# Kernel optimization log

Hardware: AMD Instinct MI355X
Metric: run time of the kernel (lower is better)

Reference implementation:

```python
import jax, jax.numpy as jnp
import numpy as np

B, N, IN_C, HEAD_C, H, EXPAND, OUT_C = 4, 2048, 256, 32, 8, 1024, 256
QKV_DIM = HEAD_C * H * 2 + IN_C * H  # 2560
LN_EPS = 1e-5


def setup_inputs() -> dict:
    key = jax.random.key(0)
    ks = jax.random.split(key, 6)
    s = lambda fan: 1.0 / np.sqrt(fan)
    return {
        "x": jax.random.normal(ks[0], (B, N, IN_C), jnp.float32),
        "ln1_g": jnp.ones((IN_C,), jnp.float32),
        "ln1_b": jnp.zeros((IN_C,), jnp.float32),
        "Wqkv": jax.random.normal(ks[1], (IN_C, QKV_DIM), jnp.float32) * s(IN_C),
        "bqkv": jnp.zeros((QKV_DIM,), jnp.float32),
        "Wm": jax.random.normal(ks[2], (IN_C * H, IN_C), jnp.float32) * s(IN_C * H),
        "bm": jnp.zeros((IN_C,), jnp.float32),
        "ln2_g": jnp.ones((IN_C,), jnp.float32),
        "ln2_b": jnp.zeros((IN_C,), jnp.float32),
        "W1": jax.random.normal(ks[3], (IN_C, EXPAND), jnp.float32) * s(IN_C),
        "b1": jnp.zeros((EXPAND,), jnp.float32),
        "W2": jax.random.normal(ks[4], (EXPAND, OUT_C), jnp.float32) * s(EXPAND),
        "b2": jnp.zeros((OUT_C,), jnp.float32),
    }


def _ln(x, g, b):
    m = x.mean(-1, keepdims=True)
    v = jnp.mean(jnp.square(x - m), axis=-1, keepdims=True)
    return (x - m) * jax.lax.rsqrt(v + LN_EPS) * g + b


def reference(x, ln1_g, ln1_b, Wqkv, bqkv, Wm, bm, ln2_g, ln2_b, W1, b1, W2, b2):
    scale = HEAD_C ** -0.5
    qkv = _ln(x, ln1_g, ln1_b) @ Wqkv + bqkv  # [B,N,QKV_DIM]
    q, k, v = jnp.split(qkv, [HEAD_C * H, 2 * HEAD_C * H], axis=-1)
    q = q.reshape(B, N, H, HEAD_C)  # H-major channel split, matches einops
    k = k.reshape(B, N, H, HEAD_C)
    v = v.reshape(B, N, H, IN_C)    # NOTE: V has in_c channels per head
    attn = jax.nn.softmax(jnp.einsum('bnhc,bmhc->bhnm', q, k) * scale, axis=-1)
    out = jnp.einsum('bhnm,bmhc->bnhc', attn, v).reshape(B, N, H * IN_C)
    x = x + out @ Wm + bm  # residual + merge-head projection
    h = jax.nn.gelu(_ln(x, ln2_g, ln2_b) @ W1 + b1, approximate=False)
    return (h @ W2 + b2) + x  # shortcut is Identity (in_c == out_c)
```

## Files before the change

### kernel.cpp

```cpp
#include <hip/hip_runtime.h>
#include <hip/hip_bf16.h>

typedef unsigned short u16;
typedef __attribute__((ext_vector_type(8))) short bf8_t;
typedef __attribute__((ext_vector_type(4))) float f4_t;
typedef __attribute__((ext_vector_type(16))) float fx16;

__device__ __forceinline__ float bf2f(u16 v) {
    union { unsigned u; float f; } c; c.u = ((unsigned)v) << 16; return c.f;
}
__device__ __forceinline__ u16 f2bf(float f) {
    union { float f; unsigned u; } c; c.f = f;
    unsigned r = 0x7FFFu + ((c.u >> 16) & 1u);
    return (u16)((c.u + r) >> 16);
}
__device__ __forceinline__ u16 f2bf_hw(float f) {
    union { __hip_bfloat16 b; u16 u; } c; c.b = __float2bfloat16(f); return c.u;
}

#define B_   4
#define N_   2048
#define INC  256
#define H_   8
#define ROWS 8192

#define SEG_X     0
#define SEG_LN1G  2097152
#define SEG_LN1B  2097408
#define SEG_WQKV  2097664
#define SEG_BQKV  2753024
#define SEG_WM    2755584
#define SEG_BM    3279872
#define SEG_LN2G  3280128
#define SEG_LN2B  3280384
#define SEG_W1    3280640
#define SEG_B1    3542784
#define SEG_W2    3543808
#define SEG_B2    3805952
#define SEG_TOT   3806208

__device__ __forceinline__ int sniff_flag(const void* x0, int t, int* sh) {
    if (t == 0) *sh = 0;
    __syncthreads();
    int bad = 0;
    #pragma unroll
    for (int k2 = 0; k2 < 4; ++k2) {
        float v = bf2f(((const u16*)x0)[t * 4 + k2]);
        if (!(fabsf(v) < 1e10f)) bad = 1;
    }
    if (bad) atomicOr(sh, 1);
    __syncthreads();
    return *sh;
}

__global__ __launch_bounds__(256) void prep_k(
    const void* p0, const void* p1, const void* p2, const void* p3, const void* p4,
    const void* p5, const void* p6, const void* p7, const void* p8, const void* p9,
    const void* p10, const void* p11, const void* p12,
    u16* __restrict__ dst, u16* __restrict__ y, int* __restrict__ mkz)
{
    const int t = threadIdx.x;
    const int blk = blockIdx.x;
    __shared__ int sflag;
    const int flag = sniff_flag(p0, t, &sflag);

    if (blk < 8192) {
        const int i = blk * 256 + t;
        float v = flag ? ((const float*)p0)[i] : bf2f(((const u16*)p0)[i]);
        dst[i] = f2bf_hw(v);
        float s = v, s2 = v * v;
        #pragma unroll
        for (int d = 1; d < 64; d <<= 1) {
            s  += __shfl_xor(s,  d, 64);
            s2 += __shfl_xor(s2, d, 64);
        }
        __shared__ float rs[8];
        int w = t >> 6;
        if ((t & 63) == 0) { rs[w] = s; rs[4 + w] = s2; }
        __syncthreads();
        s  = rs[0] + rs[1] + rs[2] + rs[3];
        s2 = rs[4] + rs[5] + rs[6] + rs[7];
        float mean = s * (1.0f / INC);
        float var  = s2 * (1.0f / INC) - mean * mean;
        float inv  = rsqrtf(var + 1e-5f);
        float g  = flag ? ((const float*)p1)[t] : bf2f(((const u16*)p1)[t]);
        float bb = flag ? ((const float*)p2)[t] : bf2f(((const u16*)p2)[t]);
        y[i] = f2bf_hw((v - mean) * inv * g + bb);
        return;
    }

    if (blk < 8210) {
        if (blk == 8192 && t < 32) mkz[t] = 0;
        const int elem = (blk - 8192) * 256 + t;
        const void* p; int j; size_t doff;
        if      (elem < 2560) { p = p4;  j = elem;        doff = SEG_BQKV + j; }
        else if (elem < 2816) { p = p6;  j = elem - 2560; doff = SEG_BM   + j; }
        else if (elem < 3072) { p = p7;  j = elem - 2816; doff = SEG_LN2G + j; }
        else if (elem < 3328) { p = p8;  j = elem - 3072; doff = SEG_LN2B + j; }
        else if (elem < 4352) { p = p10; j = elem - 3328; doff = SEG_B1   + j; }
        else                  { p = p12; j = elem - 4352; doff = SEG_B2   + j; }
        dst[doff] = flag ? f2bf(((const float*)p)[j]) : ((const u16*)p)[j];
        return;
    }

    const int blk2 = blk - 8210;
    const void* W; int Kd, Nd, kt, nt; size_t seg;
    if (blk2 < 160)      { W = p3;  Kd = 256;  Nd = 2560; kt = blk2 / 40;  nt = blk2 % 40;  seg = SEG_WQKV; }
    else if (blk2 < 288) { int i2 = blk2 - 160; W = p5;  Kd = 2048; Nd = 256;  kt = i2 >> 2;  nt = i2 & 3;  seg = SEG_WM; }
    else if (blk2 < 352) { int i2 = blk2 - 288; W = p9;  Kd = 256;  Nd = 1024; kt = i2 >> 4;  nt = i2 & 15; seg = SEG_W1; }
    else                 { int i2 = blk2 - 352; W = p11; Kd = 1024; Nd = 256;  kt = i2 >> 2;  nt = i2 & 3;  seg = SEG_W2; }
    const int k0 = kt * 64, n0 = nt * 64;

    __shared__ u16 Tl[64][66];
    #pragma unroll
    for (int p = 0; p < 16; ++p) {
        int idx = t + p * 256;
        int r = idx >> 6, c = idx & 63;
        size_t si = (size_t)(k0 + r) * Nd + n0 + c;
        Tl[r][c] = flag ? f2bf(((const float*)W)[si]) : ((const u16*)W)[si];
    }
    __syncthreads();
    u16* dp = dst + seg;
    #pragma unroll
    for (int p = 0; p < 8; ++p) {
        int idx = t + p * 256;
        int rn = idx >> 5, ck = (idx & 31) * 2;
        ushort2 v; v.x = Tl[ck][rn]; v.y = Tl[ck + 1][rn];
        *(ushort2*)(dp + (size_t)(n0 + rn) * Kd + k0 + ck) = v;
    }
}

template<bool BF16IN>
__global__ __launch_bounds__(256) void ln_k(const void* __restrict__ xp,
        const u16* __restrict__ g, const u16* __restrict__ b, u16* __restrict__ y)
{
    int row  = blockIdx.x * 4 + (threadIdx.x >> 6);
    int lane = threadIdx.x & 63;
    int c0   = lane * 4;
    float v[4];
    if (BF16IN) {
        ushort4 u = *(const ushort4*)((const u16*)xp + (size_t)row * INC + c0);
        v[0] = bf2f(u.x); v[1] = bf2f(u.y); v[2] = bf2f(u.z); v[3] = bf2f(u.w);
    } else {
        float4 f = *(const float4*)((const float*)xp + (size_t)row * INC + c0);
        v[0] = f.x; v[1] = f.y; v[2] = f.z; v[3] = f.w;
    }
    float s = v[0] + v[1] + v[2] + v[3];
    float s2 = v[0]*v[0] + v[1]*v[1] + v[2]*v[2] + v[3]*v[3];
    #pragma unroll
    for (int d = 1; d < 64; d <<= 1) {
        s  += __shfl_xor(s,  d, 64);
        s2 += __shfl_xor(s2, d, 64);
    }
    float mean = s * (1.0f / INC);
    float var  = s2 * (1.0f / INC) - mean * mean;
    float inv  = rsqrtf(var + 1e-5f);
    ushort4 gv = *(const ushort4*)(g + c0);
    ushort4 bv = *(const ushort4*)(b + c0);
    ushort4 o;
    o.x = f2bf_hw((v[0] - mean) * inv * bf2f(gv.x) + bf2f(bv.x));
    o.y = f2bf_hw((v[1] - mean) * inv * bf2f(gv.y) + bf2f(bv.y));
    o.z = f2bf_hw((v[2] - mean) * inv * bf2f(gv.z) + bf2f(bv.z));
    o.w = f2bf_hw((v[3] - mean) * inv * bf2f(gv.w) + bf2f(bv.w));
    *(ushort4*)(y + (size_t)row * INC + c0) = o;
}

enum { EP_QKV = 0, EP_MERGE = 1, EP_GELU = 2, EP_FFN2 = 3 };

template<int MODE>
__global__ __launch_bounds__(256) void gemm_big(
    const u16* __restrict__ A, const u16* __restrict__ Bt,
    const u16* __restrict__ bias, void* __restrict__ outp,
    u16* __restrict__ qh, u16* __restrict__ kh, u16* __restrict__ vh,
    int* __restrict__ mkz, int N, int K)
{
    const int t = threadIdx.x;
    const int w = t >> 6, lane = t & 63;
    const int l15 = lane & 15, quad = lane >> 4;
    const int col0 = blockIdx.x * 64;
    const int row0 = blockIdx.y * 256;
    const int mrow = row0 + w * 64;

    __shared__ u16 Tsu[256 * 72];

    const u16* Ap = A  + (size_t)(mrow + l15) * K + quad * 8;
    const u16* Bp = Bt + (size_t)(col0 + l15) * K + quad * 8;

    f4_t acc[4][4];
    #pragma unroll
    for (int mi = 0; mi < 4; ++mi)
        #pragma unroll
        for (int ni = 0; ni < 4; ++ni)
            acc[mi][ni] = (f4_t){0.f, 0.f, 0.f, 0.f};

    for (int k0 = 0; k0 < K; k0 += 32) {
        bf8_t a[4], bb[4];
        #pragma unroll
        for (int mi = 0; mi < 4; ++mi)
            a[mi] = *(const bf8_t*)(Ap + (size_t)mi * 16 * K + k0);
        #pragma unroll
        for (int ni = 0; ni < 4; ++ni)
            bb[ni] = *(const bf8_t*)(Bp + (size_t)ni * 16 * K + k0);
        #pragma unroll
        for (int ni = 0; ni < 4; ++ni)
            #pragma unroll
            for (int mi = 0; mi < 4; ++mi)
                acc[mi][ni] = __builtin_amdgcn_mfma_f32_16x16x32_bf16(
                    a[mi], bb[ni], acc[mi][ni], 0, 0, 0);
    }

    if (MODE == EP_QKV) {
        if (col0 >= 512) {
            u16 (*Ts)[268] = (u16(*)[268])Tsu;
            #pragma unroll
            for (int mi = 0; mi < 4; ++mi)
                #pragma unroll
                for (int ni = 0; ni < 4; ++ni) {
                    float bz = bf2f(bias[col0 + ni * 16 + l15]);
                    #pragma unroll
                    for (int r = 0; r < 4; ++r)
                        Ts[ni * 16 + l15][w * 64 + mi * 16 + quad * 4 + r] =
                            f2bf_hw(acc[mi][ni][r] + bz);
                }
            __syncthreads();
            int vcg = col0 - 512;
            int hh  = vcg >> 8;
            int bb2 = row0 >> 11, nb = row0 & 2047;
            int bhh = bb2 * 8 + hh;
            int tok4 = t & 3, cl = (t >> 2) & 63;
            int vc = (vcg & 255) + cl;
            #pragma unroll
            for (int kb = 0; kb < 16; ++kb) {
                u16* dp = vh + (((size_t)bhh * 128 + ((nb >> 4) + kb)) * 256 + vc) * 16 + tok4 * 4;
                *(ushort4*)dp = *(const ushort4*)&Ts[cl][kb * 16 + tok4 * 4];
            }
        } else if (col0 < 256) {
            #pragma unroll
            for (int mi = 0; mi < 4; ++mi)
                #pragma unroll
                for (int r = 0; r < 4; ++r) {
                    int rg = mrow + mi * 16 + quad * 4 + r;
                    int bb2 = rg >> 11, n = rg & 2047;
                    #pragma unroll
                    for (int ni = 0; ni < 4; ++ni) {
                        int col = col0 + ni * 16 + l15;
                        float v = acc[mi][ni][r] + bf2f(bias[col]);
                        qh[(((size_t)(bb2 * 8 + (col >> 5))) * 2048 + n) * 32 + (col & 31)] = f2bf_hw(v);
                    }
                }
        } else {
            const int hA  = (col0 - 256) >> 5;
            const int bb2 = row0 >> 11;
            float mxA = 0.f, mxB = 0.f;
            #pragma unroll
            for (int mi = 0; mi < 4; ++mi)
                #pragma unroll
                for (int r = 0; r < 4; ++r) {
                    int rg = mrow + mi * 16 + quad * 4 + r;
                    int n = rg & 2047;
                    float vv[4];
                    #pragma unroll
                    for (int ni = 0; ni < 4; ++ni) {
                        int col = col0 + ni * 16 + l15;
                        float v = acc[mi][ni][r] + bf2f(bias[col]);
                        vv[ni] = v;
                        int c2 = col - 256;
                        int hd = c2 >> 5, ch = c2 & 31;
                        kh[(((size_t)(bb2 * 8 + hd) * 64 + (n >> 5)) * 2 + (ch >> 4)) * 512
                           + (n & 31) * 16 + (ch & 15)] = f2bf_hw(v);
                    }
                    float sA = vv[0] * vv[0] + vv[1] * vv[1];
                    float sB = vv[2] * vv[2] + vv[3] * vv[3];
                    #pragma unroll
                    for (int d = 1; d < 16; d <<= 1) {
                        sA += __shfl_xor(sA, d, 64);
                        sB += __shfl_xor(sB, d, 64);
                    }
                    mxA = fmaxf(mxA, sA);
                    mxB = fmaxf(mxB, sB);
                }
            if ((lane & 15) == 0) {
                atomicMax(mkz + bb2 * 8 + hA,     __float_as_int(mxA));
                atomicMax(mkz + bb2 * 8 + hA + 1, __float_as_int(mxB));
            }
        }
    } else {
        u16 (*Ts2)[72] = (u16(*)[72])Tsu;
        float bz[4];
        #pragma unroll
        for (int ni = 0; ni < 4; ++ni) bz[ni] = bf2f(bias[col0 + ni * 16 + l15]);
        #pragma unroll
        for (int mi = 0; mi < 4; ++mi)
            #pragma unroll
            for (int ni = 0; ni < 4; ++ni)
                #pragma unroll
                for (int r = 0; r < 4; ++r) {
                    float v = acc[mi][ni][r] + bz[ni];
                    v = 0.5f * v * (1.0f + erff(v * 0.70710678118654752f));
                    Ts2[w * 64 + mi * 16 + quad * 4 + r][ni * 16 + l15] = f2bf_hw(v);
                }
        __syncthreads();
        const int rl0 = t >> 3, c8 = (t & 7) * 8;
        #pragma unroll
        for (int p = 0; p < 8; ++p) {
            int rl = rl0 + p * 32;
            *(bf8_t*)((u16*)outp + (size_t)(row0 + rl) * N + col0 + c8) =
                *(const bf8_t*)&Ts2[rl][c8];
        }
    }
}

template<int MODE>
__global__ __launch_bounds__(256) void gemm_mfma(
    const u16* __restrict__ A, const u16* __restrict__ Bt,
    const u16* __restrict__ bias, const void* __restrict__ res,
    void* __restrict__ outp, int N, int K)
{
    const int t = threadIdx.x;
    const int w = t >> 6, lane = t & 63;
    const int l15 = lane & 15, quad = lane >> 4;
    const int col0 = blockIdx.x * 64;
    const int row0 = blockIdx.y * 128;
    const int mrow = row0 + w * 32;

    __shared__ float Tf[128][68];

    const u16* Ap = A  + (size_t)(mrow + l15) * K + quad * 8;
    const u16* Bp = Bt + (size_t)(col0 + l15) * K + quad * 8;

    f4_t acc[2][4];
    #pragma unroll
    for (int mi = 0; mi < 2; ++mi)
        #pragma unroll
        for (int ni = 0; ni < 4; ++ni)
            acc[mi][ni] = (f4_t){0.f, 0.f, 0.f, 0.f};

    for (int k0 = 0; k0 < K; k0 += 64) {
        bf8_t a[2][2], bb[4][2];
        #pragma unroll
        for (int kc = 0; kc < 2; ++kc) {
            #pragma unroll
            for (int mi = 0; mi < 2; ++mi)
                a[mi][kc] = *(const bf8_t*)(Ap + (size_t)mi * 16 * K + k0 + kc * 32);
            #pragma unroll
            for (int ni = 0; ni < 4; ++ni)
                bb[ni][kc] = *(const bf8_t*)(Bp + (size_t)ni * 16 * K + k0 + kc * 32);
        }
        #pragma unroll
        for (int kc = 0; kc < 2; ++kc)
            #pragma unroll
            for (int ni = 0; ni < 4; ++ni)
                #pragma unroll
                for (int mi = 0; mi < 2; ++mi)
                    acc[mi][ni] = __builtin_amdgcn_mfma_f32_16x16x32_bf16(
                        a[mi][kc], bb[ni][kc], acc[mi][ni], 0, 0, 0);
    }

    float bz[4];
    #pragma unroll
    for (int ni = 0; ni < 4; ++ni) bz[ni] = bf2f(bias[col0 + ni * 16 + l15]);
    #pragma unroll
    for (int mi = 0; mi < 2; ++mi)
        #pragma unroll
        for (int ni = 0; ni < 4; ++ni)
            #pragma unroll
            for (int r = 0; r < 4; ++r)
                Tf[w * 32 + mi * 16 + quad * 4 + r][ni * 16 + l15] = acc[mi][ni][r] + bz[ni];
    __syncthreads();

    const int rl0 = t >> 4, c4 = (t & 15) * 4;
    #pragma unroll
    for (int p = 0; p < 8; ++p) {
        int rl = rl0 + p * 16;
        float4 v = *(const float4*)&Tf[rl][c4];
        size_t base = (size_t)(row0 + rl) * N + col0 + c4;
        if (MODE == EP_MERGE) {
            ushort4 rv = *(const ushort4*)((const u16*)res + base);
            v.x += bf2f(rv.x); v.y += bf2f(rv.y); v.z += bf2f(rv.z); v.w += bf2f(rv.w);
        } else {
            float4 rv = *(const float4*)((const float*)res + base);
            v.x += rv.x; v.y += rv.y; v.z += rv.z; v.w += rv.w;
        }
        *(float4*)((float*)outp + base) = v;
    }
}

__global__ __launch_bounds__(256) void attn_k(
    const u16* __restrict__ qh, const u16* __restrict__ kh,
    const u16* __restrict__ vhT, const float* __restrict__ mk2,
    u16* __restrict__ ao)
{
    const int t = threadIdx.x;
    const int w = t >> 6, lane = t & 63;
    const int l31 = lane & 31, hi = lane >> 5;
    const int id = blockIdx.x;
    const int qt = (id >> 3) & 31;
    const int bh = (id >> 8) * 8 + (id & 7);
    const int b  = bh >> 3, h = bh & 7;
    const int n0 = qt * 64;
    const float SCALE = 0.17677669529663687f;
    const int sw = (l31 & 7) << 4;

    __shared__ __align__(16) u16 Pb[2][64][128];
    __shared__ float lds_l[4][64];
    __shared__ float lds_t[64];

    bf8_t qf[2][2];
    #pragma unroll
    for (int m = 0; m < 2; ++m)
        #pragma unroll
        for (int ks = 0; ks < 2; ++ks)
            qf[m][ks] = *(const bf8_t*)(qh + ((size_t)bh * 2048 + n0 + m * 32 + l31) * 32
                                        + ks * 16 + hi * 8);

    float mrow[2];
    #pragma unroll
    for (int m = 0; m < 2; ++m) {
        float q2 = 0.f;
        #pragma unroll
        for (int ks = 0; ks < 2; ++ks)
            #pragma unroll
            for (int i = 0; i < 8; ++i) {
                float qv = bf2f((u16)qf[m][ks][i]); q2 += qv * qv;
            }
        q2 += __shfl_xor(q2, 32, 64);
        mrow[m] = SCALE * sqrtf(q2 * mk2[bh]);
    }

    fx16 acc[2][2];
    #pragma unroll
    for (int a1 = 0; a1 < 2; ++a1)
        #pragma unroll
        for (int a2 = 0; a2 < 2; ++a2)
            #pragma unroll
            for (int e = 0; e < 16; ++e) acc[a1][a2][e] = 0.f;
    float lsum[2] = {0.f, 0.f};

    fx16 z16;
    #pragma unroll
    for (int e = 0; e < 16; ++e) z16[e] = 0.f;

    auto finish = [&](const fx16& s, int m, int g, char* base) {
        float p0 = __expf(fmaf(s[4 * g + 0], SCALE, -mrow[m]));
        float p1 = __expf(fmaf(s[4 * g + 1], SCALE, -mrow[m]));
        float p2 = __expf(fmaf(s[4 * g + 2], SCALE, -mrow[m]));
        float p3 = __expf(fmaf(s[4 * g + 3], SCALE, -mrow[m]));
        lsum[m] += (p0 + p1) + (p2 + p3);
        ushort4 pk;
        pk.x = f2bf_hw(p0); pk.y = f2bf_hw(p1); pk.z = f2bf_hw(p2); pk.w = f2bf_hw(p3);
        *(ushort4*)(base + (m * 32 + l31) * 256 + ((w * 64 + 16 * g + 8 * hi) ^ sw)) = pk;
    };

    bf8_t kA0, kA1;
    auto ldK = [&](int c) {
        const u16* kp = kh + ((size_t)bh * 64 + c * 4 + w) * 1024 + l31 * 16 + hi * 8;
        kA0 = *(const bf8_t*)kp;
        kA1 = *(const bf8_t*)(kp + 512);
    };

    {
        ldK(0);
        fx16 sA = __builtin_amdgcn_mfma_f32_32x32x16_bf16(kA0, qf[0][0], z16, 0, 0, 0);
        sA = __builtin_amdgcn_mfma_f32_32x32x16_bf16(kA1, qf[0][1], sA, 0, 0, 0);
        fx16 sB = __builtin_amdgcn_mfma_f32_32x32x16_bf16(kA0, qf[1][0], z16, 0, 0, 0);
        sB = __builtin_amdgcn_mfma_f32_32x32x16_bf16(kA1, qf[1][1], sB, 0, 0, 0);
        ldK(1);
        char* base0 = (char*)&Pb[0][0][0];
        #pragma unroll
        for (int g = 0; g < 4; ++g) finish(sA, 0, g, base0);
        #pragma unroll
        for (int g = 0; g < 4; ++g) finish(sB, 1, g, base0);
    }

    const u16* vpb = vhT + (((size_t)bh * 128) * 256 + w * 64 + l31) * 16 + hi * 8;
    bf8_t vb0 = *(const bf8_t*)vpb;
    bf8_t vb1 = *(const bf8_t*)(vpb + 512);

    int buf = 0;
    for (int c = 0; c < 16; ++c, buf ^= 1) {
        __syncthreads();
        const bool qn = (c < 15);
        fx16 sA, sB;
        if (qn) {
            sA = __builtin_amdgcn_mfma_f32_32x32x16_bf16(kA0, qf[0][0], z16, 0, 0, 0);
            sA = __builtin_amdgcn_mfma_f32_32x32x16_bf16(kA1, qf[0][1], sA, 0, 0, 0);
        }
        const char* pb = (const char*)&Pb[buf][0][0];
        char* wr = (char*)&Pb[buf ^ 1][0][0];
        const u16* vp = vpb + (size_t)c * 32768;
        #pragma unroll
        for (int ks = 0; ks < 8; ++ks) {
            bf8_t nv0 = *(const bf8_t*)(vp + (ks + 1) * 4096);
            bf8_t nv1 = *(const bf8_t*)(vp + (ks + 1) * 4096 + 512);
            bf8_t pa0 = *(const bf8_t*)(pb + l31 * 256        + ((ks * 32 + hi * 16) ^ sw));
            bf8_t pa1 = *(const bf8_t*)(pb + (32 + l31) * 256 + ((ks * 32 + hi * 16) ^ sw));
            __builtin_amdgcn_s_setprio(1);
            acc[0][0] = __builtin_amdgcn_mfma_f32_32x32x16_bf16(pa0, vb0, acc[0][0], 0, 0, 0);
            acc[0][1] = __builtin_amdgcn_mfma_f32_32x32x16_bf16(pa0, vb1, acc[0][1], 0, 0, 0);
            acc[1][0] = __builtin_amdgcn_mfma_f32_32x32x16_bf16(pa1, vb0, acc[1][0], 0, 0, 0);
            acc[1][1] = __builtin_amdgcn_mfma_f32_32x32x16_bf16(pa1, vb1, acc[1][1], 0, 0, 0);
            __builtin_amdgcn_s_setprio(0);
            if (qn) {
                if (ks < 4) {
                    finish(sA, 0, ks, wr);
                    if (ks == 3) {
                        sB = __builtin_amdgcn_mfma_f32_32x32x16_bf16(kA0, qf[1][0], z16, 0, 0, 0);
                        sB = __builtin_amdgcn_mfma_f32_32x32x16_bf16(kA1, qf[1][1], sB, 0, 0, 0);
                        if (c < 14) ldK(c + 2);
                    }
                } else {
                    finish(sB, 1, ks - 4, wr);
                }
            }
            vb0 = nv0; vb1 = nv1;
        }
    }

    #pragma unroll
    for (int m = 0; m < 2; ++m) {
        lsum[m] += __shfl_xor(lsum[m], 32, 64);
        if (hi == 0) lds_l[w][m * 32 + l31] = lsum[m];
    }
    __syncthreads();
    if (t < 64) lds_t[t] = lds_l[0][t] + lds_l[1][t] + lds_l[2][t] + lds_l[3][t];
    __syncthreads();

    #pragma unroll
    for (int mt = 0; mt < 2; ++mt)
        #pragma unroll
        for (int g = 0; g < 4; ++g) {
            f4_t lv = *(const f4_t*)&lds_t[mt * 32 + 8 * g + 4 * hi];
            #pragma unroll
            for (int j = 0; j < 4; ++j) {
                float inv = 1.0f / lv[j];
                int q = mt * 32 + 8 * g + 4 * hi + j;
                size_t rowbase = ((size_t)(b * 2048 + n0 + q)) * 2048 + h * 256 + w * 64;
                #pragma unroll
                for (int nt = 0; nt < 2; ++nt)
                    ao[rowbase + nt * 32 + l31] = f2bf_hw(acc[mt][nt][g * 4 + j] * inv);
            }
        }
}

extern "C" void kernel_launch(void* const* d_in, const int* in_sizes, int n_in,
                              void* d_out, int out_size, void* d_ws, size_t ws_size,
                              hipStream_t stream)
{
    u16* wsu = (u16*)d_ws;
    float* mk = (float*)(wsu + 64);

    const size_t CVT0 = 128;
    const size_t Y0   = CVT0 + SEG_TOT;
    const size_t QH0  = Y0  + 2097152;
    const size_t KH0  = QH0 + 2097152;
    const size_t VT0  = KH0 + 2097152;
    const size_t AO0  = VT0 + 16777216;
    const size_t X20  = AO0 + 16777216;

    u16* cvt = wsu + CVT0;
    u16* y   = wsu + Y0;
    u16* qh  = wsu + QH0;
    u16* kh  = wsu + KH0;
    u16* vhT = wsu + VT0;
    u16* ao  = wsu + AO0;
    float* x2 = (float*)(wsu + X20);
    u16* hbb  = wsu + AO0;

    const u16* xc   = cvt + SEG_X;
    const u16* Wqkv = cvt + SEG_WQKV;
    const u16* bqkv = cvt + SEG_BQKV;
    const u16* Wm   = cvt + SEG_WM;
    const u16* bm   = cvt + SEG_BM;
    const u16* ln2g = cvt + SEG_LN2G;
    const u16* ln2b = cvt + SEG_LN2B;
    const u16* W1   = cvt + SEG_W1;
    const u16* b1   = cvt + SEG_B1;
    const u16* W2   = cvt + SEG_W2;
    const u16* b2   = cvt + SEG_B2;

    prep_k<<<8626, 256, 0, stream>>>(
        d_in[0], d_in[1], d_in[2], d_in[3], d_in[4], d_in[5], d_in[6],
        d_in[7], d_in[8], d_in[9], d_in[10], d_in[11], d_in[12],
        cvt, y, (int*)mk);

    gemm_big<EP_QKV><<<dim3(2560 / 64, ROWS / 256), 256, 0, stream>>>(
        y, Wqkv, bqkv, nullptr, qh, kh, vhT, (int*)mk, 2560, 256);
    attn_k<<<1024, 256, 0, stream>>>(qh, kh, vhT, mk, ao);
    gemm_mfma<EP_MERGE><<<dim3(256 / 64, ROWS / 128), 256, 0, stream>>>(
        ao, Wm, bm, xc, x2, 256, 2048);
    ln_k<false><<<ROWS / 4, 256, 0, stream>>>(x2, ln2g, ln2b, y);
    gemm_big<EP_GELU><<<dim3(1024 / 64, ROWS / 256), 256, 0, stream>>>(
        y, W1, b1, hbb, nullptr, nullptr, nullptr, nullptr, 1024, 256);
    gemm_mfma<EP_FFN2><<<dim3(256 / 64, ROWS / 128), 256, 0, stream>>>(
        hbb, W2, b2, x2, d_out, 256, 1024);
}
```

Measured before the change: 331.2 us.

## Stage GEMM operand tiles in LDS via direct global-to-LDS loads with swizzle

Both GEMM kernels now load A and B tiles cooperatively into shared memory with global_load_lds (16-byte direct loads) using an XOR swizzle, then read MFMA fragments from LDS. Previously each wave loaded its fragments straight from global memory, so the B tile was fetched redundantly by every wave. The change aims to cut redundant global traffic and improve coalescing. In exchange it adds two barriers per K step with no double buffering, so load latency is not overlapped with compute.

```diff
diff --git a/kernel.cpp b/kernel.cpp
--- a/kernel.cpp
+++ b/kernel.cpp
@@ -16,6 +16,12 @@
 }
 __device__ __forceinline__ u16 f2bf_hw(float f) {
     union { __hip_bfloat16 b; u16 u; } c; c.b = __float2bfloat16(f); return c.u;
+}
+
+typedef __attribute__((address_space(3))) unsigned as3_u32;
+typedef __attribute__((address_space(1))) const unsigned as1_u32;
+__device__ __forceinline__ void gl16(const u16* g, u16* l) {
+    __builtin_amdgcn_global_load_lds((as1_u32*)(const void*)g, (as3_u32*)(void*)l, 16, 0, 0);
 }
 
 #define B_   4
@@ -179,12 +185,12 @@
     const int l15 = lane & 15, quad = lane >> 4;
     const int col0 = blockIdx.x * 64;
     const int row0 = blockIdx.y * 256;
-    const int mrow = row0 + w * 64;
-
-    __shared__ u16 Tsu[256 * 72];
-
-    const u16* Ap = A  + (size_t)(mrow + l15) * K + quad * 8;
-    const u16* Bp = Bt + (size_t)(col0 + l15) * K + quad * 8;
+    const int lr = lane >> 3;
+    const int sc = ((lane & 7) ^ lr) * 8;
+
+    __shared__ __align__(16) u16 Sb[20480];
+    u16* Al = Sb;
+    u16* Bl = Sb + 16384;
 
     f4_t acc[4][4];
     #pragma unroll
@@ -193,25 +199,42 @@
         for (int ni = 0; ni < 4; ++ni)
             acc[mi][ni] = (f4_t){0.f, 0.f, 0.f, 0.f};
 
-    for (int k0 = 0; k0 < K; k0 += 32) {
-        bf8_t a[4], bb[4];
-        #pragma unroll
-        for (int mi = 0; mi < 4; ++mi)
-            a[mi] = *(const bf8_t*)(Ap + (size_t)mi * 16 * K + k0);
-        #pragma unroll
-        for (int ni = 0; ni < 4; ++ni)
-            bb[ni] = *(const bf8_t*)(Bp + (size_t)ni * 16 * K + k0);
-        #pragma unroll
-        for (int ni = 0; ni < 4; ++ni)
-            #pragma unroll
-            for (int mi = 0; mi < 4; ++mi)
-                acc[mi][ni] = __builtin_amdgcn_mfma_f32_16x16x32_bf16(
-                    a[mi], bb[ni], acc[mi][ni], 0, 0, 0);
-    }
+    for (int k0 = 0; k0 < K; k0 += 64) {
+        #pragma unroll
+        for (int i = 0; i < 8; ++i) {
+            int r = w * 64 + i * 8;
+            gl16(A + (size_t)(row0 + r + lr) * K + k0 + sc, Al + r * 64);
+        }
+        gl16(Bt + (size_t)(col0 + w * 16 + lr) * K + k0 + sc,     Bl + (w * 16) * 64);
+        gl16(Bt + (size_t)(col0 + w * 16 + 8 + lr) * K + k0 + sc, Bl + (w * 16 + 8) * 64);
+        __syncthreads();
+        #pragma unroll
+        for (int kc = 0; kc < 2; ++kc) {
+            bf8_t a[4], bb[4];
+            #pragma unroll
+            for (int mi = 0; mi < 4; ++mi) {
+                int row = w * 64 + mi * 16 + l15;
+                a[mi] = *(const bf8_t*)(Al + row * 64 + ((kc * 4 + quad) ^ (row & 7)) * 8);
+            }
+            #pragma unroll
+            for (int ni = 0; ni < 4; ++ni) {
+                int row = ni * 16 + l15;
+                bb[ni] = *(const bf8_t*)(Bl + row * 64 + ((kc * 4 + quad) ^ (row & 7)) * 8);
+            }
+            #pragma unroll
+            for (int ni = 0; ni < 4; ++ni)
+                #pragma unroll
+                for (int mi = 0; mi < 4; ++mi)
+                    acc[mi][ni] = __builtin_amdgcn_mfma_f32_16x16x32_bf16(
+                        a[mi], bb[ni], acc[mi][ni], 0, 0, 0);
+        }
+        __syncthreads();
+    }
+    const int mrow = row0 + w * 64;
 
     if (MODE == EP_QKV) {
         if (col0 >= 512) {
-            u16 (*Ts)[268] = (u16(*)[268])Tsu;
+            u16 (*Ts)[268] = (u16(*)[268])Sb;
             #pragma unroll
             for (int mi = 0; mi < 4; ++mi)
                 #pragma unroll
@@ -285,7 +308,7 @@
             }
         }
     } else {
-        u16 (*Ts2)[72] = (u16(*)[72])Tsu;
+        u16 (*Ts2)[72] = (u16(*)[72])Sb;
         float bz[4];
         #pragma unroll
         for (int ni = 0; ni < 4; ++ni) bz[ni] = bf2f(bias[col0 + ni * 16 + l15]);
@@ -321,12 +344,13 @@
     const int l15 = lane & 15, quad = lane >> 4;
     const int col0 = blockIdx.x * 64;
     const int row0 = blockIdx.y * 128;
-    const int mrow = row0 + w * 32;
-
-    __shared__ float Tf[128][68];
-
-    const u16* Ap = A  + (size_t)(mrow + l15) * K + quad * 8;
-    const u16* Bp = Bt + (size_t)(col0 + l15) * K + quad * 8;
+    const int lr = lane >> 3;
+    const int sc = ((lane & 7) ^ lr) * 8;
+
+    __shared__ __align__(16) float SBf[8704];
+    u16* Al = (u16*)SBf;
+    u16* Bl = (u16*)SBf + 8192;
+    float (*Tf)[68] = (float(*)[68])SBf;
 
     f4_t acc[2][4];
     #pragma unroll
@@ -336,24 +360,35 @@
             acc[mi][ni] = (f4_t){0.f, 0.f, 0.f, 0.f};
 
     for (int k0 = 0; k0 < K; k0 += 64) {
-        bf8_t a[2][2], bb[4][2];
+        #pragma unroll
+        for (int i = 0; i < 4; ++i) {
+            int r = w * 32 + i * 8;
+            gl16(A + (size_t)(row0 + r + lr) * K + k0 + sc, Al + r * 64);
+        }
+        gl16(Bt + (size_t)(col0 + w * 16 + lr) * K + k0 + sc,     Bl + (w * 16) * 64);
+        gl16(Bt + (size_t)(col0 + w * 16 + 8 + lr) * K + k0 + sc, Bl + (w * 16 + 8) * 64);
+        __syncthreads();
         #pragma unroll
         for (int kc = 0; kc < 2; ++kc) {
-            #pragma unroll
-            for (int mi = 0; mi < 2; ++mi)
-                a[mi][kc] = *(const bf8_t*)(Ap + (size_t)mi * 16 * K + k0 + kc * 32);
-            #pragma unroll
-            for (int ni = 0; ni < 4; ++ni)
-                bb[ni][kc] = *(const bf8_t*)(Bp + (size_t)ni * 16 * K + k0 + kc * 32);
-        }
-        #pragma unroll
-        for (int kc = 0; kc < 2; ++kc)
+            bf8_t a[2], bb[4];
+            #pragma unroll
+            for (int mi = 0; mi < 2; ++mi) {
+                int row = w * 32 + mi * 16 + l15;
+                a[mi] = *(const bf8_t*)(Al + row * 64 + ((kc * 4 + quad) ^ (row & 7)) * 8);
+            }
+            #pragma unroll
+            for (int ni = 0; ni < 4; ++ni) {
+                int row = ni * 16 + l15;
+                bb[ni] = *(const bf8_t*)(Bl + row * 64 + ((kc * 4 + quad) ^ (row & 7)) * 8);
+            }
             #pragma unroll
             for (int ni = 0; ni < 4; ++ni)
                 #pragma unroll
                 for (int mi = 0; mi < 2; ++mi)
                     acc[mi][ni] = __builtin_amdgcn_mfma_f32_16x16x32_bf16(
-                        a[mi][kc], bb[ni][kc], acc[mi][ni], 0, 0, 0);
+                        a[mi], bb[ni], acc[mi][ni], 0, 0, 0);
+        }
+        __syncthreads();
     }
 
     float bz[4];
```

After: 294.8 us. 11.0% less time.
